# Performance work log

Hardware: AMD Instinct MI355X
Metric: run time of the kernel (lower is better)

The kernel has to match this reference:

```python
import jax, jax.numpy as jnp
import numpy as np

B, T, C = 256, 512, 256
K = 8  # number of distinct phoneme classes used (indices into phoneme_inventory)
# weights dict {'aa':2.0,'ae':0.5,'ah':1.5,'ao':1.2,'aw':0.8}, rest default 1.0,
# materialized as a dense per-class-index weight vector:
WEIGHTS = np.ones(K, dtype=np.float32)
WEIGHTS[:5] = [2.0, 0.5, 1.5, 1.2, 0.8]


def setup_inputs() -> dict:
    key = jax.random.key(0)
    k1, k2 = jax.random.split(key)
    embeddings = jax.random.normal(k1, (B, T, C), dtype=jnp.float32)
    phonemes = jax.random.randint(k2, (B, T), 0, K, dtype=jnp.int64)
    weights = jnp.asarray(WEIGHTS)
    return {"embeddings": embeddings, "phonemes": phonemes, "weights": weights}


def reference(embeddings, phonemes, weights):
    Bs, Ts, Cs = embeddings.shape
    # F.normalize(p=2, dim=-1) with eps=1e-12
    norm = jnp.linalg.norm(embeddings, axis=-1, keepdims=True)
    emb = embeddings / jnp.maximum(norm, 1e-12)
    # all-pairs cosine similarity per timestep: [T, B, B]
    exp_sim = jnp.exp(jnp.einsum('itc,jtc->tij', emb, emb))
    eye = jnp.eye(Bs, dtype=bool)  # [B, B]
    p = phonemes.T  # [T, B]
    pos = (p[:, :, None] == p[:, None, :]) & ~eye  # [T, B, B]
    num = jnp.where(pos, exp_sim, 0.0).sum(-1)          # [T, B]
    den = jnp.where(~eye, exp_sim, 0.0).sum(-1)          # [T, B]
    per_sample = -jnp.log(num / (den + 1e-6))            # [T, B]
    # segment-mean per (timestep, class), then weighted mean over present classes
    oh = jax.nn.one_hot(p, weights.shape[0], dtype=per_sample.dtype)  # [T, B, K]
    counts = oh.sum(1)                                   # [T, K]
    sums = jnp.einsum('tb,tbk->tk', per_sample, oh)      # [T, K]
    present = counts > 0
    class_mean = sums / jnp.maximum(counts, 1.0)
    loss_t = jnp.where(present, class_mean * weights, 0.0).sum(-1) / present.sum(-1)
    return loss_t.mean()
```

## Files before the change

kernel.cpp:

```cpp
#include <hip/hip_runtime.h>

#define Bn 256
#define Tn 512
#define Cn 256
#define Kn 8

typedef __attribute__((ext_vector_type(4))) float f32x4;

__global__ __launch_bounds__(512, 4)
void tcon_k(const float* __restrict__ emb,
            const int* __restrict__ phon,
            const float* __restrict__ wts,
            float* __restrict__ out) {
    __shared__ __align__(16) unsigned char Esh[Bn * Bn];
    __shared__ float invn[Bn];
    __shared__ int   pcls[Bn];
    __shared__ float num_s[Bn], den_s[Bn];
    __shared__ float csum[Kn];
    __shared__ int   ccnt[Kn];

    const int t    = blockIdx.x;
    const int tid  = threadIdx.x;
    const int lane = tid & 63;
    const int wave = tid >> 6;

    if (tid < Kn) { csum[tid] = 0.0f; ccnt[tid] = 0; }
    if (tid < Bn) pcls[tid] = phon[tid * Tn + t];

    #pragma unroll 4
    for (int it = 0; it < 16; ++it) {
        const int f   = tid + it * 512;
        const int row = f >> 5;
        const int b   = f & 31;
        const float4* p = (const float4*)(emb + ((size_t)row * Tn + t) * Cn);
        const float4 v0 = p[2 * b];
        const float4 v1 = p[2 * b + 1];
        int lo = __builtin_amdgcn_cvt_pk_fp8_f32(v0.x, v0.y, 0, false);
        lo     = __builtin_amdgcn_cvt_pk_fp8_f32(v0.z, v0.w, lo, true);
        int hi = __builtin_amdgcn_cvt_pk_fp8_f32(v1.x, v1.y, 0, false);
        hi     = __builtin_amdgcn_cvt_pk_fp8_f32(v1.z, v1.w, hi, true);
        const int q  = b & 3;
        const int kk = b >> 2;
        const int kp = kk >> 1;
        const int addr = row * 256 + ((((q << 2) + kp) ^ (row & 7)) << 4)
                       + ((kk & 1) << 3);
        int2 pk; pk.x = lo; pk.y = hi;
        *(int2*)&Esh[addr] = pk;
    }
    __syncthreads();

    const int q   = lane >> 4;
    const int l15 = lane & 15;
    const int e3  = l15 & 7;
    const int i0  = wave * 32;
    const int sd  = wave >> 1;

    f32x4 acc[2][4];

#define ZERO_ACC() do {                                                      \
    _Pragma("unroll") for (int _m = 0; _m < 2; ++_m)                         \
    _Pragma("unroll") for (int _n = 0; _n < 4; ++_n)                         \
        acc[_m][_n] = (f32x4){0.f, 0.f, 0.f, 0.f};                           \
} while (0)

#define COMPUTE_STRIP(JB) do {                                               \
    ZERO_ACC();                                                              \
    _Pragma("unroll") for (int kp = 0; kp < 4; ++kp) {                       \
        const int sw = (((q << 2) + kp) ^ e3) << 4;                          \
        ulonglong2 _a[2], _b[4];                                             \
        _Pragma("unroll") for (int _m = 0; _m < 2; ++_m)                     \
            _a[_m] = *(const ulonglong2*)&Esh[(i0 + _m * 16 + l15) * 256 + sw]; \
        _Pragma("unroll") for (int _n = 0; _n < 4; ++_n)                     \
            _b[_n] = *(const ulonglong2*)&Esh[((JB) + _n * 16 + l15) * 256 + sw]; \
        _Pragma("unroll") for (int _m = 0; _m < 2; ++_m)                     \
        _Pragma("unroll") for (int _n = 0; _n < 4; ++_n) {                   \
            acc[_m][_n] = __builtin_amdgcn_mfma_f32_16x16x32_fp8_fp8(        \
                (long)_a[_m].x, (long)_b[_n].x, acc[_m][_n], 0, 0, 0);       \
            acc[_m][_n] = __builtin_amdgcn_mfma_f32_16x16x32_fp8_fp8(        \
                (long)_a[_m].y, (long)_b[_n].y, acc[_m][_n], 0, 0, 0);       \
        }                                                                    \
    }                                                                        \
} while (0)

#define EPILOGUE(JB) do {                                                    \
    _Pragma("unroll") for (int _n = 0; _n < 4; ++_n) {                       \
        const int _j  = (JB) + _n * 16 + l15;                                \
        const int _pj = pcls[_j];                                            \
        const float _ij = invn[_j];                                          \
        _Pragma("unroll") for (int _m = 0; _m < 2; ++_m)                     \
        _Pragma("unroll") for (int _r = 0; _r < 4; ++_r) {                   \
            const int _e = _m * 4 + _r;                                      \
            const int _ir = i0 + _m * 16 + q * 4 + _r;                       \
            const float _ex = __expf(acc[_m][_n][_r] * inv_i[_e] * _ij);     \
            const bool _nd = (_ir != _j);                                    \
            den_p[_e] += _nd ? _ex : 0.0f;                                   \
            num_p[_e] += (_nd && (_pj == pi[_e])) ? _ex : 0.0f;              \
        }                                                                    \
    }                                                                        \
} while (0)

    COMPUTE_STRIP(sd * 64);
    if ((wave & 1) == 0) {
        #pragma unroll
        for (int r = 0; r < 4; ++r)
            if (l15 == q * 4 + r) {
                invn[i0 + l15]      = rsqrtf(fmaxf(acc[0][0][r], 1e-24f));
                invn[i0 + 16 + l15] = rsqrtf(fmaxf(acc[1][1][r], 1e-24f));
            }
    } else {
        #pragma unroll
        for (int r = 0; r < 4; ++r)
            if (l15 == q * 4 + r) {
                invn[i0 + l15]      = rsqrtf(fmaxf(acc[0][2][r], 1e-24f));
                invn[i0 + 16 + l15] = rsqrtf(fmaxf(acc[1][3][r], 1e-24f));
            }
    }
    __syncthreads();

    float num_p[8], den_p[8], inv_i[8];
    int   pi[8];
    #pragma unroll
    for (int e = 0; e < 8; ++e) {
        const int irow = i0 + (e >> 2) * 16 + q * 4 + (e & 3);
        num_p[e] = 0.0f; den_p[e] = 0.0f;
        pi[e]    = pcls[irow];
        inv_i[e] = invn[irow];
    }

    EPILOGUE(sd * 64);
    for (int s = 0; s < 4; ++s) {
        if (s == sd) continue;
        COMPUTE_STRIP(s * 64);
        EPILOGUE(s * 64);
    }

    #pragma unroll
    for (int e = 0; e < 8; ++e) {
        float n = num_p[e], d = den_p[e];
        #pragma unroll
        for (int m = 1; m <= 8; m <<= 1) {
            n += __shfl_xor(n, m, 64);
            d += __shfl_xor(d, m, 64);
        }
        if (l15 == e) {
            const int irow = i0 + (e >> 2) * 16 + q * 4 + (e & 3);
            num_s[irow] = n;
            den_s[irow] = d;
        }
    }
    __syncthreads();

    if (tid < Bn) {
        const float ps = __logf(den_s[tid] + 1e-6f) - __logf(num_s[tid]);
        atomicAdd(&csum[pcls[tid]], ps);
        atomicAdd(&ccnt[pcls[tid]], 1);
    }
    __syncthreads();

    if (tid == 0) {
        float accv = 0.0f; int np = 0;
        #pragma unroll
        for (int k = 0; k < Kn; ++k)
            if (ccnt[k] > 0) { accv += (csum[k] / (float)ccnt[k]) * wts[k]; ++np; }
        atomicAdd(out, (accv / (float)np) * (1.0f / (float)Tn));
    }
#undef ZERO_ACC
#undef COMPUTE_STRIP
#undef EPILOGUE
}

extern "C" void kernel_launch(void* const* d_in, const int* in_sizes, int n_in,
                              void* d_out, int out_size, void* d_ws, size_t ws_size,
                              hipStream_t stream) {
    const float* emb  = (const float*)d_in[0];
    const int*   phon = (const int*)d_in[1];
    const float* wts  = (const float*)d_in[2];
    float*       out  = (float*)d_out;

    hipMemsetAsync(out, 0, sizeof(float), stream);
    tcon_k<<<Tn, 512, 0, stream>>>(emb, phon, wts, out);
}
```

Measured before the change: 206.6 us.

## Process two timesteps per block with double-buffered LDS prefetch

Each block now handles two consecutive timesteps with 1024 threads. The second timestep's embeddings are converted to fp8 and staged into a second LDS buffer while the first timestep's MFMA strips and epilogue run. Column strips are split between wave pairs, with num/den partials combined through shared memory. This aims to hide global-load latency behind compute. In exchange it doubles LDS per block and halves the grid, which cuts resident blocks per CU and may reduce the overlap the hardware already got from running multiple blocks.

```diff
diff --git a/kernel.cpp b/kernel.cpp
--- a/kernel.cpp
+++ b/kernel.cpp
@@ -7,53 +7,60 @@
 
 typedef __attribute__((ext_vector_type(4))) float f32x4;
 
-__global__ __launch_bounds__(512, 4)
+__global__ __launch_bounds__(1024, 4)
 void tcon_k(const float* __restrict__ emb,
             const int* __restrict__ phon,
             const float* __restrict__ wts,
             float* __restrict__ out) {
-    __shared__ __align__(16) unsigned char Esh[Bn * Bn];
+    __shared__ __align__(16) unsigned char Esh[2][Bn * Bn];
     __shared__ float invn[Bn];
-    __shared__ int   pcls[Bn];
-    __shared__ float num_s[Bn], den_s[Bn];
+    __shared__ int   pcls[2][Bn];
+    __shared__ float num_s[2][Bn], den_s[2][Bn];
     __shared__ float csum[Kn];
     __shared__ int   ccnt[Kn];
 
-    const int t    = blockIdx.x;
+    const int t0   = blockIdx.x * 2;
+    const int t1   = t0 + 1;
     const int tid  = threadIdx.x;
     const int lane = tid & 63;
     const int wave = tid >> 6;
+    const int rg   = wave >> 1;
+    const int sh   = wave & 1;
+    const int i0   = rg * 32;
+    const int sd   = rg >> 1;
+    const bool own = ((rg >> 2) == sh);
+    const int fs   = own ? sd : (sh << 1);
+    const int os   = own ? (sd ^ 1) : ((sh << 1) | 1);
+
+    const int q   = lane >> 4;
+    const int l15 = lane & 15;
+    const int e3  = l15 & 7;
 
     if (tid < Kn) { csum[tid] = 0.0f; ccnt[tid] = 0; }
-    if (tid < Bn) pcls[tid] = phon[tid * Tn + t];
+    if (tid < Bn) {
+        pcls[0][tid] = phon[tid * Tn + t0];
+        pcls[1][tid] = phon[tid * Tn + t1];
+    }
 
     #pragma unroll 4
-    for (int it = 0; it < 16; ++it) {
-        const int f   = tid + it * 512;
+    for (int it = 0; it < 8; ++it) {
+        const int f   = tid + it * 1024;
         const int row = f >> 5;
         const int b   = f & 31;
-        const float4* p = (const float4*)(emb + ((size_t)row * Tn + t) * Cn);
+        const float4* p = (const float4*)(emb + ((size_t)row * Tn + t0) * Cn);
         const float4 v0 = p[2 * b];
         const float4 v1 = p[2 * b + 1];
         int lo = __builtin_amdgcn_cvt_pk_fp8_f32(v0.x, v0.y, 0, false);
         lo     = __builtin_amdgcn_cvt_pk_fp8_f32(v0.z, v0.w, lo, true);
         int hi = __builtin_amdgcn_cvt_pk_fp8_f32(v1.x, v1.y, 0, false);
         hi     = __builtin_amdgcn_cvt_pk_fp8_f32(v1.z, v1.w, hi, true);
-        const int q  = b & 3;
-        const int kk = b >> 2;
-        const int kp = kk >> 1;
-        const int addr = row * 256 + ((((q << 2) + kp) ^ (row & 7)) << 4)
-                       + ((kk & 1) << 3);
+        const int qq = b & 3, kk = b >> 2, kp = kk >> 1;
+        const int ad = row * 256 + ((((qq << 2) + kp) ^ (row & 7)) << 4)
+                     + ((kk & 1) << 3);
         int2 pk; pk.x = lo; pk.y = hi;
-        *(int2*)&Esh[addr] = pk;
+        *(int2*)&Esh[0][ad] = pk;
     }
     __syncthreads();
-
-    const int q   = lane >> 4;
-    const int l15 = lane & 15;
-    const int e3  = l15 & 7;
-    const int i0  = wave * 32;
-    const int sd  = wave >> 1;
 
     f32x4 acc[2][4];
 
@@ -61,6 +68,26 @@
     _Pragma("unroll") for (int _m = 0; _m < 2; ++_m)                         \
     _Pragma("unroll") for (int _n = 0; _n < 4; ++_n)                         \
         acc[_m][_n] = (f32x4){0.f, 0.f, 0.f, 0.f};                           \
+} while (0)
+
+#define STAGE4(ITBASE) do {                                                  \
+    _Pragma("unroll") for (int _it = (ITBASE); _it < (ITBASE) + 4; ++_it) {  \
+        const int _f   = tid + _it * 1024;                                   \
+        const int _row = _f >> 5;                                            \
+        const int _b   = _f & 31;                                            \
+        const float4* _p = (const float4*)(emb + ((size_t)_row * Tn + t1) * Cn); \
+        const float4 _v0 = _p[2 * _b];                                       \
+        const float4 _v1 = _p[2 * _b + 1];                                   \
+        int _lo = __builtin_amdgcn_cvt_pk_fp8_f32(_v0.x, _v0.y, 0, false);   \
+        _lo     = __builtin_amdgcn_cvt_pk_fp8_f32(_v0.z, _v0.w, _lo, true);  \
+        int _hi = __builtin_amdgcn_cvt_pk_fp8_f32(_v1.x, _v1.y, 0, false);   \
+        _hi     = __builtin_amdgcn_cvt_pk_fp8_f32(_v1.z, _v1.w, _hi, true);  \
+        const int _qq = _b & 3, _kk = _b >> 2, _kp = _kk >> 1;               \
+        const int _ad = _row * 256 + ((((_qq << 2) + _kp) ^ (_row & 7)) << 4)\
+                      + ((_kk & 1) << 3);                                    \
+        int2 _pk; _pk.x = _lo; _pk.y = _hi;                                  \
+        *(int2*)&Esh[1][_ad] = _pk;                                          \
+    }                                                                        \
 } while (0)
 
 #define COMPUTE_STRIP(JB) do {                                               \
@@ -69,9 +96,9 @@
         const int sw = (((q << 2) + kp) ^ e3) << 4;                          \
         ulonglong2 _a[2], _b[4];                                             \
         _Pragma("unroll") for (int _m = 0; _m < 2; ++_m)                     \
-            _a[_m] = *(const ulonglong2*)&Esh[(i0 + _m * 16 + l15) * 256 + sw]; \
+            _a[_m] = *(const ulonglong2*)&Esh[tt][(i0 + _m * 16 + l15) * 256 + sw]; \
         _Pragma("unroll") for (int _n = 0; _n < 4; ++_n)                     \
-            _b[_n] = *(const ulonglong2*)&Esh[((JB) + _n * 16 + l15) * 256 + sw]; \
+            _b[_n] = *(const ulonglong2*)&Esh[tt][((JB) + _n * 16 + l15) * 256 + sw]; \
         _Pragma("unroll") for (int _m = 0; _m < 2; ++_m)                     \
         _Pragma("unroll") for (int _n = 0; _n < 4; ++_n) {                   \
             acc[_m][_n] = __builtin_amdgcn_mfma_f32_16x16x32_fp8_fp8(        \
@@ -85,7 +112,7 @@
 #define EPILOGUE(JB) do {                                                    \
     _Pragma("unroll") for (int _n = 0; _n < 4; ++_n) {                       \
         const int _j  = (JB) + _n * 16 + l15;                                \
-        const int _pj = pcls[_j];                                            \
+        const int _pj = pcls[tt][_j];                                        \
         const float _ij = invn[_j];                                          \
         _Pragma("unroll") for (int _m = 0; _m < 2; ++_m)                     \
         _Pragma("unroll") for (int _r = 0; _r < 4; ++_r) {                   \
@@ -99,72 +126,82 @@
     }                                                                        \
 } while (0)
 
-    COMPUTE_STRIP(sd * 64);
-    if ((wave & 1) == 0) {
+    #pragma unroll
+    for (int tt = 0; tt < 2; ++tt) {
+        COMPUTE_STRIP(fs * 64);
+        if (own) {
+            if ((rg & 1) == 0) {
+                #pragma unroll
+                for (int r = 0; r < 4; ++r)
+                    if (l15 == q * 4 + r) {
+                        invn[i0 + l15]      = rsqrtf(fmaxf(acc[0][0][r], 1e-24f));
+                        invn[i0 + 16 + l15] = rsqrtf(fmaxf(acc[1][1][r], 1e-24f));
+                    }
+            } else {
+                #pragma unroll
+                for (int r = 0; r < 4; ++r)
+                    if (l15 == q * 4 + r) {
+                        invn[i0 + l15]      = rsqrtf(fmaxf(acc[0][2][r], 1e-24f));
+                        invn[i0 + 16 + l15] = rsqrtf(fmaxf(acc[1][3][r], 1e-24f));
+                    }
+            }
+        }
+        if (tt == 0) STAGE4(0);
+        __syncthreads();
+
+        float num_p[8], den_p[8], inv_i[8];
+        int   pi[8];
         #pragma unroll
-        for (int r = 0; r < 4; ++r)
-            if (l15 == q * 4 + r) {
-                invn[i0 + l15]      = rsqrtf(fmaxf(acc[0][0][r], 1e-24f));
-                invn[i0 + 16 + l15] = rsqrtf(fmaxf(acc[1][1][r], 1e-24f));
-            }
-    } else {
+        for (int e = 0; e < 8; ++e) {
+            const int irow = i0 + (e >> 2) * 16 + q * 4 + (e & 3);
+            num_p[e] = 0.0f; den_p[e] = 0.0f;
+            pi[e]    = pcls[tt][irow];
+            inv_i[e] = invn[irow];
+        }
+
+        EPILOGUE(fs * 64);
+        if (tt == 0) STAGE4(4);
+        COMPUTE_STRIP(os * 64);
+        EPILOGUE(os * 64);
+
         #pragma unroll
-        for (int r = 0; r < 4; ++r)
-            if (l15 == q * 4 + r) {
-                invn[i0 + l15]      = rsqrtf(fmaxf(acc[0][2][r], 1e-24f));
-                invn[i0 + 16 + l15] = rsqrtf(fmaxf(acc[1][3][r], 1e-24f));
-            }
-    }
-    __syncthreads();
-
-    float num_p[8], den_p[8], inv_i[8];
-    int   pi[8];
-    #pragma unroll
-    for (int e = 0; e < 8; ++e) {
-        const int irow = i0 + (e >> 2) * 16 + q * 4 + (e & 3);
-        num_p[e] = 0.0f; den_p[e] = 0.0f;
-        pi[e]    = pcls[irow];
-        inv_i[e] = invn[irow];
-    }
-
-    EPILOGUE(sd * 64);
-    for (int s = 0; s < 4; ++s) {
-        if (s == sd) continue;
-        COMPUTE_STRIP(s * 64);
-        EPILOGUE(s * 64);
-    }
-
-    #pragma unroll
-    for (int e = 0; e < 8; ++e) {
-        float n = num_p[e], d = den_p[e];
-        #pragma unroll
-        for (int m = 1; m <= 8; m <<= 1) {
-            n += __shfl_xor(n, m, 64);
-            d += __shfl_xor(d, m, 64);
-        }
-        if (l15 == e) {
-            const int irow = i0 + (e >> 2) * 16 + q * 4 + (e & 3);
-            num_s[irow] = n;
-            den_s[irow] = d;
-        }
-    }
-    __syncthreads();
-
-    if (tid < Bn) {
-        const float ps = __logf(den_s[tid] + 1e-6f) - __logf(num_s[tid]);
-        atomicAdd(&csum[pcls[tid]], ps);
-        atomicAdd(&ccnt[pcls[tid]], 1);
-    }
-    __syncthreads();
-
-    if (tid == 0) {
-        float accv = 0.0f; int np = 0;
-        #pragma unroll
-        for (int k = 0; k < Kn; ++k)
-            if (ccnt[k] > 0) { accv += (csum[k] / (float)ccnt[k]) * wts[k]; ++np; }
-        atomicAdd(out, (accv / (float)np) * (1.0f / (float)Tn));
+        for (int e = 0; e < 8; ++e) {
+            float n = num_p[e], d = den_p[e];
+            #pragma unroll
+            for (int m = 1; m <= 8; m <<= 1) {
+                n += __shfl_xor(n, m, 64);
+                d += __shfl_xor(d, m, 64);
+            }
+            if (l15 == e) {
+                const int irow = i0 + (e >> 2) * 16 + q * 4 + (e & 3);
+                num_s[sh][irow] = n;
+                den_s[sh][irow] = d;
+            }
+        }
+        __syncthreads();
+
+        if (tid < Bn) {
+            const float nn = num_s[0][tid] + num_s[1][tid];
+            const float dd = den_s[0][tid] + den_s[1][tid];
+            const float ps = __logf(dd + 1e-6f) - __logf(nn);
+            const int c = pcls[tt][tid];
+            atomicAdd(&csum[c], ps);
+            atomicAdd(&ccnt[c], 1);
+        }
+        __syncthreads();
+
+        if (tid == 0) {
+            float accv = 0.0f; int np = 0;
+            #pragma unroll
+            for (int k = 0; k < Kn; ++k) {
+                if (ccnt[k] > 0) { accv += (csum[k] / (float)ccnt[k]) * wts[k]; ++np; }
+                csum[k] = 0.0f; ccnt[k] = 0;
+            }
+            atomicAdd(out, (accv / (float)np) * (1.0f / (float)Tn));
+        }
     }
 #undef ZERO_ACC
+#undef STAGE4
 #undef COMPUTE_STRIP
 #undef EPILOGUE
 }
@@ -178,5 +215,5 @@
     float*       out  = (float*)d_out;
 
     hipMemsetAsync(out, 0, sizeof(float), stream);
-    tcon_k<<<Tn, 512, 0, stream>>>(emb, phon, wts, out);
+    tcon_k<<<Tn / 2, 1024, 0, stream>>>(emb, phon, wts, out);
 }
```

Result: slower. 226.6 us (+9.7%).

## Hoist A fragments into registers and process 32-column strips with smaller accumulators

Applied to the files above, without the earlier changes.

Each wave now loads its 32-row A fragments from LDS once into registers and keeps them for all column strips, instead of reloading them per strip. The j loop goes over eight 32-wide strips in XOR order, fully unrolled, with a 2x2 accumulator tile instead of 2x4. The diagonal strip computes the norms directly. The launch bound is switched to amdgpu_waves_per_eu(4,4). This cuts repeated LDS reads of A and lowers accumulator register pressure, but each strip now does fewer MFMAs per B load and the full unroll grows code size.

```diff
diff --git a/kernel.cpp b/kernel.cpp
--- a/kernel.cpp
+++ b/kernel.cpp
@@ -7,7 +7,8 @@
 
 typedef __attribute__((ext_vector_type(4))) float f32x4;
 
-__global__ __launch_bounds__(512, 4)
+__global__ __launch_bounds__(512)
+__attribute__((amdgpu_waves_per_eu(4, 4)))
 void tcon_k(const float* __restrict__ emb,
             const int* __restrict__ phon,
             const float* __restrict__ wts,
@@ -23,6 +24,11 @@
     const int tid  = threadIdx.x;
     const int lane = tid & 63;
     const int wave = tid >> 6;
+    const int i0   = wave * 32;
+
+    const int q   = lane >> 4;
+    const int l15 = lane & 15;
+    const int e3  = l15 & 7;
 
     if (tid < Kn) { csum[tid] = 0.0f; ccnt[tid] = 0; }
     if (tid < Bn) pcls[tid] = phon[tid * Tn + t];
@@ -39,51 +45,37 @@
         lo     = __builtin_amdgcn_cvt_pk_fp8_f32(v0.z, v0.w, lo, true);
         int hi = __builtin_amdgcn_cvt_pk_fp8_f32(v1.x, v1.y, 0, false);
         hi     = __builtin_amdgcn_cvt_pk_fp8_f32(v1.z, v1.w, hi, true);
-        const int q  = b & 3;
-        const int kk = b >> 2;
-        const int kp = kk >> 1;
-        const int addr = row * 256 + ((((q << 2) + kp) ^ (row & 7)) << 4)
-                       + ((kk & 1) << 3);
+        const int qq = b & 3, kk = b >> 2, kp = kk >> 1;
+        const int ad = row * 256 + ((((qq << 2) + kp) ^ (row & 7)) << 4)
+                     + ((kk & 1) << 3);
         int2 pk; pk.x = lo; pk.y = hi;
-        *(int2*)&Esh[addr] = pk;
+        *(int2*)&Esh[ad] = pk;
     }
     __syncthreads();
 
-    const int q   = lane >> 4;
-    const int l15 = lane & 15;
-    const int e3  = l15 & 7;
-    const int i0  = wave * 32;
-    const int sd  = wave >> 1;
+    f32x4 acc[2][2];
 
-    f32x4 acc[2][4];
-
-#define ZERO_ACC() do {                                                      \
+#define COMPUTE_HALF(JB) do {                                                \
     _Pragma("unroll") for (int _m = 0; _m < 2; ++_m)                         \
-    _Pragma("unroll") for (int _n = 0; _n < 4; ++_n)                         \
+    _Pragma("unroll") for (int _n = 0; _n < 2; ++_n)                         \
         acc[_m][_n] = (f32x4){0.f, 0.f, 0.f, 0.f};                           \
-} while (0)
-
-#define COMPUTE_STRIP(JB) do {                                               \
-    ZERO_ACC();                                                              \
-    _Pragma("unroll") for (int kp = 0; kp < 4; ++kp) {                       \
-        const int sw = (((q << 2) + kp) ^ e3) << 4;                          \
-        ulonglong2 _a[2], _b[4];                                             \
+    _Pragma("unroll") for (int _kp = 0; _kp < 4; ++_kp) {                    \
+        const int _sw = (((q << 2) + _kp) ^ e3) << 4;                        \
+        ulonglong2 _b[2];                                                    \
+        _Pragma("unroll") for (int _n = 0; _n < 2; ++_n)                     \
+            _b[_n] = *(const ulonglong2*)&Esh[((JB) + _n * 16 + l15) * 256 + _sw]; \
         _Pragma("unroll") for (int _m = 0; _m < 2; ++_m)                     \
-            _a[_m] = *(const ulonglong2*)&Esh[(i0 + _m * 16 + l15) * 256 + sw]; \
-        _Pragma("unroll") for (int _n = 0; _n < 4; ++_n)                     \
-            _b[_n] = *(const ulonglong2*)&Esh[((JB) + _n * 16 + l15) * 256 + sw]; \
-        _Pragma("unroll") for (int _m = 0; _m < 2; ++_m)                     \
-        _Pragma("unroll") for (int _n = 0; _n < 4; ++_n) {                   \
+        _Pragma("unroll") for (int _n = 0; _n < 2; ++_n) {                   \
             acc[_m][_n] = __builtin_amdgcn_mfma_f32_16x16x32_fp8_fp8(        \
-                (long)_a[_m].x, (long)_b[_n].x, acc[_m][_n], 0, 0, 0);       \
+                (long)a_[_kp][_m].x, (long)_b[_n].x, acc[_m][_n], 0, 0, 0);  \
             acc[_m][_n] = __builtin_amdgcn_mfma_f32_16x16x32_fp8_fp8(        \
-                (long)_a[_m].y, (long)_b[_n].y, acc[_m][_n], 0, 0, 0);       \
+                (long)a_[_kp][_m].y, (long)_b[_n].y, acc[_m][_n], 0, 0, 0);  \
         }                                                                    \
     }                                                                        \
 } while (0)
 
 #define EPILOGUE(JB) do {                                                    \
-    _Pragma("unroll") for (int _n = 0; _n < 4; ++_n) {                       \
+    _Pragma("unroll") for (int _n = 0; _n < 2; ++_n) {                       \
         const int _j  = (JB) + _n * 16 + l15;                                \
         const int _pj = pcls[_j];                                            \
         const float _ij = invn[_j];                                          \
@@ -99,22 +91,21 @@
     }                                                                        \
 } while (0)
 
-    COMPUTE_STRIP(sd * 64);
-    if ((wave & 1) == 0) {
+    ulonglong2 a_[4][2];
+    #pragma unroll
+    for (int kp = 0; kp < 4; ++kp)
         #pragma unroll
-        for (int r = 0; r < 4; ++r)
-            if (l15 == q * 4 + r) {
-                invn[i0 + l15]      = rsqrtf(fmaxf(acc[0][0][r], 1e-24f));
-                invn[i0 + 16 + l15] = rsqrtf(fmaxf(acc[1][1][r], 1e-24f));
-            }
-    } else {
-        #pragma unroll
-        for (int r = 0; r < 4; ++r)
-            if (l15 == q * 4 + r) {
-                invn[i0 + l15]      = rsqrtf(fmaxf(acc[0][2][r], 1e-24f));
-                invn[i0 + 16 + l15] = rsqrtf(fmaxf(acc[1][3][r], 1e-24f));
-            }
-    }
+        for (int m = 0; m < 2; ++m)
+            a_[kp][m] = *(const ulonglong2*)
+                &Esh[(i0 + m * 16 + l15) * 256 + ((((q << 2) + kp) ^ e3) << 4)];
+
+    COMPUTE_HALF(i0);
+    #pragma unroll
+    for (int r = 0; r < 4; ++r)
+        if (l15 == q * 4 + r) {
+            invn[i0 + l15]      = rsqrtf(fmaxf(acc[0][0][r], 1e-24f));
+            invn[i0 + 16 + l15] = rsqrtf(fmaxf(acc[1][1][r], 1e-24f));
+        }
     __syncthreads();
 
     float num_p[8], den_p[8], inv_i[8];
@@ -127,11 +118,12 @@
         inv_i[e] = invn[irow];
     }
 
-    EPILOGUE(sd * 64);
-    for (int s = 0; s < 4; ++s) {
-        if (s == sd) continue;
-        COMPUTE_STRIP(s * 64);
-        EPILOGUE(s * 64);
+    EPILOGUE(i0);
+    #pragma unroll
+    for (int k = 1; k < 8; ++k) {
+        const int jb = (wave ^ k) * 32;
+        COMPUTE_HALF(jb);
+        EPILOGUE(jb);
     }
 
     #pragma unroll
@@ -164,8 +156,7 @@
             if (ccnt[k] > 0) { accv += (csum[k] / (float)ccnt[k]) * wts[k]; ++np; }
         atomicAdd(out, (accv / (float)np) * (1.0f / (float)Tn));
     }
-#undef ZERO_ACC
-#undef COMPUTE_STRIP
+#undef COMPUTE_HALF
 #undef EPILOGUE
 }
 
```

New measurement: 265.4 us. 1.28x slower.
